# Performance work log

Measured on AMD Instinct MI355X. Metric: run time of the kernel, lower is better.

Reference implementation:

```python
import jax, jax.numpy as jnp
import numpy as np

D_MODEL = 1024
N_HEADS = 16
HEAD_DIM = D_MODEL // N_HEADS


def setup_inputs() -> dict:
    key = jax.random.key(0)
    k_x, k_qkv, k_out = jax.random.split(key, 3)
    B, T = 4, 2048
    x = jax.random.normal(k_x, (B, T, D_MODEL), dtype=jnp.float32)
    # Linear(bias=False): y = x @ W, with W stored as [in, out]
    W_qkv = jax.random.normal(k_qkv, (D_MODEL, 3 * D_MODEL), dtype=jnp.float32) * (D_MODEL ** -0.5)
    W_out = jax.random.normal(k_out, (D_MODEL, D_MODEL), dtype=jnp.float32) * (D_MODEL ** -0.5)
    return {"x": x, "W_qkv": W_qkv, "W_out": W_out}


def reference(x, W_qkv, W_out):
    B, T, C = x.shape
    H, Dh = N_HEADS, HEAD_DIM
    scale = 1.0 / jnp.sqrt(jnp.asarray(Dh, dtype=x.dtype))

    qkv = x @ W_qkv  # [B,T,3C]
    q, k, v = jnp.split(qkv, 3, axis=-1)

    def split_heads(t):
        return t.reshape(B, T, H, Dh).transpose(0, 2, 1, 3)  # [B,H,T,Dh]

    q, k, v = split_heads(q), split_heads(k), split_heads(v)

    scores = jnp.einsum('bhqd,bhkd->bhqk', q, k) * scale  # [B,H,T,T]
    causal = jnp.tril(jnp.ones((T, T), dtype=bool))
    scores = jnp.where(causal, scores, jnp.asarray(-jnp.inf, dtype=scores.dtype))
    attn = jax.nn.softmax(scores, axis=-1)
    # dropout p=0.0 -> identity
    out = jnp.einsum('bhqk,bhkd->bhqd', attn, v)  # [B,H,T,Dh]
    out = out.transpose(0, 2, 1, 3).reshape(B, T, C)
    return out @ W_out
```

## Files before the change

kernel.cpp:

```cpp
#include <hip/hip_runtime.h>
#include <stdint.h>

typedef unsigned short u16;
typedef float f32x4 __attribute__((ext_vector_type(4)));
typedef short s16x8 __attribute__((ext_vector_type(8)));

#define SEQ 2048
#define DM 1024
#define NH 16
#define HD 64
#define BATCH 4
#define ROWS (BATCH*SEQ)

__device__ __forceinline__ u16 f32_bf16(float f) {
  union { float f; uint32_t u; } c; c.f = f;
  uint32_t u = c.u;
  return (u16)((u + 0x7fffu + ((u >> 16) & 1u)) >> 16);
}
__device__ __forceinline__ u16 f32_bf16_trunc(float f) {
  union { float f; uint32_t u; } c; c.f = f;
  return (u16)(c.u >> 16);
}

#define GLOAD_LDS16(g, l) __builtin_amdgcn_global_load_lds( \
    (__attribute__((address_space(1))) void*)(g),           \
    (__attribute__((address_space(3))) void*)(l), 16, 0, 0)

__global__ __launch_bounds__(256) void cast_bf16_k(const float* __restrict__ in,
                                                   u16* __restrict__ out, int n4) {
  int i = blockIdx.x * 256 + threadIdx.x;
  if (i >= n4) return;
  float4 v = ((const float4*)in)[i];
  ushort4 o;
  o.x = f32_bf16(v.x); o.y = f32_bf16(v.y); o.z = f32_bf16(v.z); o.w = f32_bf16(v.w);
  ((ushort4*)out)[i] = o;
}

__global__ __launch_bounds__(256) void cast_transpose_k(const float* __restrict__ in,
                                                        u16* __restrict__ out, int R, int C) {
  __shared__ float tile[32][33];
  int c0 = blockIdx.x * 32, r0 = blockIdx.y * 32;
  int t = threadIdx.x;
  int lr = t >> 3, lc = (t & 7) * 4;
  float4 v = *(const float4*)(in + (size_t)(r0 + lr) * C + c0 + lc);
  tile[lr][lc] = v.x; tile[lr][lc + 1] = v.y; tile[lr][lc + 2] = v.z; tile[lr][lc + 3] = v.w;
  __syncthreads();
  ushort4 o;
  o.x = f32_bf16(tile[lc + 0][lr]);
  o.y = f32_bf16(tile[lc + 1][lr]);
  o.z = f32_bf16(tile[lc + 2][lr]);
  o.w = f32_bf16(tile[lc + 3][lr]);
  *(ushort4*)(out + (size_t)(c0 + lr) * R + r0 + lc) = o;
}

#define QSCALE 0.18033688011112042f


__device__ __forceinline__ f32x4 mfma16(s16x8 a, s16x8 b, f32x4 c) {
  return __builtin_amdgcn_mfma_f32_16x16x32_bf16(a, b, c, 0, 0, 0);
}

template<int STG, int ENDVM, int LAST>
__device__ __forceinline__ void tile_step(
    const u16* lAc, const u16* lBc,
    const u16* lAn, const u16* lBn,
    u16* lAs, u16* lBs,
    const u16* gA0, const u16* gA1, const u16* gB0, const u16* gB1,
    int d0, int d1, int aoff, int boff,
    s16x8 (&fa)[4], s16x8 (&fb)[4],
    s16x8 (&na)[4], s16x8 (&nb)[4],
    f32x4 (&acc)[8][4])
{
  __builtin_amdgcn_s_barrier();
  __builtin_amdgcn_sched_barrier(0);
  s16x8 f1[4];
#pragma unroll
  for (int mi = 0; mi < 4; ++mi) f1[mi] = *(const s16x8*)&lAc[aoff + 2048 + mi * 512];
  if (STG) { GLOAD_LDS16(gA0, lAs + d0); GLOAD_LDS16(gA1, lAs + d1); }
  asm volatile("s_waitcnt lgkmcnt(4)" ::: "memory");
  __builtin_amdgcn_sched_barrier(0);
  __builtin_amdgcn_s_setprio(1);
#pragma unroll
  for (int mi = 0; mi < 4; ++mi)
#pragma unroll
    for (int ni = 0; ni < 4; ++ni)
      acc[mi][ni] = mfma16(fa[mi], fb[ni], acc[mi][ni]);
  __builtin_amdgcn_s_setprio(0);
  __builtin_amdgcn_sched_barrier(0);
  if (STG) { GLOAD_LDS16(gB0, lBs + d0); GLOAD_LDS16(gB1, lBs + d1); }
  if (ENDVM == 8)      asm volatile("s_waitcnt vmcnt(8)" ::: "memory");
  else if (ENDVM == 4) asm volatile("s_waitcnt vmcnt(4)" ::: "memory");
  else if (ENDVM == 0) asm volatile("s_waitcnt vmcnt(0)" ::: "memory");
  __builtin_amdgcn_s_barrier();
  __builtin_amdgcn_sched_barrier(0);
  if (!LAST) {
#pragma unroll
    for (int ni = 0; ni < 4; ++ni) nb[ni] = *(const s16x8*)&lBn[boff + ni * 512];
#pragma unroll
    for (int mi = 0; mi < 4; ++mi) na[mi] = *(const s16x8*)&lAn[aoff + mi * 512];
    asm volatile("s_waitcnt lgkmcnt(8)" ::: "memory");
  } else {
    asm volatile("s_waitcnt lgkmcnt(0)" ::: "memory");
  }
  __builtin_amdgcn_sched_barrier(0);
  __builtin_amdgcn_s_setprio(1);
#pragma unroll
  for (int mi = 0; mi < 4; ++mi)
#pragma unroll
    for (int ni = 0; ni < 4; ++ni)
      acc[4 + mi][ni] = mfma16(f1[mi], fb[ni], acc[4 + mi][ni]);
  __builtin_amdgcn_s_setprio(0);
  __builtin_amdgcn_sched_barrier(0);
}

__global__ __launch_bounds__(512, 2) void qkv_gemm(
    const u16* __restrict__ A, const u16* __restrict__ Bt,
    u16* __restrict__ Qo, u16* __restrict__ Ko, u16* __restrict__ Vo)
{
  __shared__ u16 lA[4][8192];
  __shared__ u16 lB[4][8192];
  int t = threadIdx.x;

  int flat = blockIdx.y * 12 + blockIdx.x;
  int swz = (flat & 7) * 48 + (flat >> 3);
  int by = swz / 12, bx = swz - by * 12;
  int m0 = by * 256, n0 = bx * 256;

  int lane = t & 63, w = t >> 6;
  int m16 = lane & 15, quad = lane >> 4;
  int wm = w >> 2, wn = w & 3;

  int r0 = t >> 2;
  int scol = ((t & 3) ^ ((t >> 3) & 3)) * 8;
  const u16* Ag0 = A  + (size_t)(m0 + r0) * DM + scol;
  const u16* Ag1 = A  + (size_t)(m0 + 128 + r0) * DM + scol;
  const u16* Bg0 = Bt + (size_t)(n0 + r0) * DM + scol;
  const u16* Bg1 = Bt + (size_t)(n0 + 128 + r0) * DM + scol;
  int d0 = t * 8, d1 = 4096 + t * 8;

  int ka = (quad ^ ((m16 >> 1) & 3)) * 8;
  int aoff = (wm * 128 + m16) * 32 + ka;
  int boff = (wn * 64 + m16) * 32 + ka;

  f32x4 acc[8][4];
#pragma unroll
  for (int mi = 0; mi < 8; ++mi)
#pragma unroll
    for (int ni = 0; ni < 4; ++ni)
#pragma unroll
      for (int r = 0; r < 4; ++r) acc[mi][ni][r] = 0.f;

#pragma unroll
  for (int kt = 0; kt < 3; ++kt) {
    GLOAD_LDS16(Ag0 + kt * 32, lA[kt] + d0);
    GLOAD_LDS16(Ag1 + kt * 32, lA[kt] + d1);
    GLOAD_LDS16(Bg0 + kt * 32, lB[kt] + d0);
    GLOAD_LDS16(Bg1 + kt * 32, lB[kt] + d1);
  }
  asm volatile("s_waitcnt vmcnt(8)" ::: "memory");
  __builtin_amdgcn_s_barrier();
  __builtin_amdgcn_sched_barrier(0);

  s16x8 fa0[4], fb0[4], fa1[4], fb1[4];
#pragma unroll
  for (int ni = 0; ni < 4; ++ni) fb0[ni] = *(const s16x8*)&lB[0][boff + ni * 512];
#pragma unroll
  for (int mi = 0; mi < 4; ++mi) fa0[mi] = *(const s16x8*)&lA[0][aoff + mi * 512];

  for (int it = 0; it < 14; ++it) {
    int T = 2 * it;
    tile_step<1, 8, 0>(lA[T & 3], lB[T & 3], lA[(T + 1) & 3], lB[(T + 1) & 3],
                       lA[(T + 3) & 3], lB[(T + 3) & 3],
                       Ag0 + (T + 3) * 32, Ag1 + (T + 3) * 32,
                       Bg0 + (T + 3) * 32, Bg1 + (T + 3) * 32,
                       d0, d1, aoff, boff, fa0, fb0, fa1, fb1, acc);
    tile_step<1, 8, 0>(lA[(T + 1) & 3], lB[(T + 1) & 3], lA[(T + 2) & 3], lB[(T + 2) & 3],
                       lA[(T + 4) & 3], lB[(T + 4) & 3],
                       Ag0 + (T + 4) * 32, Ag1 + (T + 4) * 32,
                       Bg0 + (T + 4) * 32, Bg1 + (T + 4) * 32,
                       d0, d1, aoff, boff, fa1, fb1, fa0, fb0, acc);
  }
  tile_step<1, 8, 0>(lA[0], lB[0], lA[1], lB[1], lA[3], lB[3],
                     Ag0 + 31 * 32, Ag1 + 31 * 32, Bg0 + 31 * 32, Bg1 + 31 * 32,
                     d0, d1, aoff, boff, fa0, fb0, fa1, fb1, acc);
  tile_step<0, 4, 0>(lA[1], lB[1], lA[2], lB[2], lA[0], lB[0],
                     Ag0, Ag1, Bg0, Bg1, d0, d1, aoff, boff, fa1, fb1, fa0, fb0, acc);
  tile_step<0, 0, 0>(lA[2], lB[2], lA[3], lB[3], lA[0], lB[0],
                     Ag0, Ag1, Bg0, Bg1, d0, d1, aoff, boff, fa0, fb0, fa1, fb1, acc);
  tile_step<0, -1, 1>(lA[3], lB[3], lA[0], lB[0], lA[0], lB[0],
                      Ag0, Ag1, Bg0, Bg1, d0, d1, aoff, boff, fa1, fb1, fa0, fb0, acc);

#pragma unroll
  for (int mi = 0; mi < 8; ++mi) {
    int gr = m0 + wm * 128 + mi * 16 + quad * 4;
    int b = gr >> 11, tt = gr & 2047;
#pragma unroll
    for (int ni = 0; ni < 4; ++ni) {
      int gc = n0 + wn * 64 + ni * 16 + m16;
      int sec = gc >> 10, rem = gc & 1023, h = rem >> 6, d = rem & 63;
      if (sec == 0) {
#pragma unroll
        for (int r = 0; r < 4; ++r)
          Qo[(((size_t)b * NH + h) * SEQ + tt + r) * HD + d] = f32_bf16(acc[mi][ni][r] * QSCALE);
      } else if (sec == 1) {
#pragma unroll
        for (int r = 0; r < 4; ++r)
          Ko[(((size_t)b * NH + h) * SEQ + tt + r) * HD + d] = f32_bf16(acc[mi][ni][r]);
      } else {
        ushort4 o;
        o.x = f32_bf16(acc[mi][ni][0]); o.y = f32_bf16(acc[mi][ni][1]);
        o.z = f32_bf16(acc[mi][ni][2]); o.w = f32_bf16(acc[mi][ni][3]);
        *(ushort4*)&Vo[(((size_t)b * NH + h) * HD + d) * SEQ + tt] = o;
      }
    }
  }
}

template<int EPI>
__global__ __launch_bounds__(256) void gemm_bt(
    const u16* __restrict__ A, const u16* __restrict__ Bt,
    float* __restrict__ Cf, u16* __restrict__ Qo, u16* __restrict__ Ko, u16* __restrict__ Vo,
    int M, int N, int K)
{
  __shared__ u16 As[128 * 32];
  __shared__ u16 Bs[128 * 32];
  int t = threadIdx.x;
  int m0 = blockIdx.y * 128, n0 = blockIdx.x * 128;

  int srow = t >> 2, scol8 = (t & 3) * 8;
  const u16* Ag0 = A  + (size_t)(m0 + srow) * K + scol8;
  const u16* Ag1 = A  + (size_t)(m0 + 64 + srow) * K + scol8;
  const u16* Bg0 = Bt + (size_t)(n0 + srow) * K + scol8;
  const u16* Bg1 = Bt + (size_t)(n0 + 64 + srow) * K + scol8;
  u16* Al0 = As + t * 8;  u16* Al1 = As + 2048 + t * 8;
  u16* Bl0 = Bs + t * 8;  u16* Bl1 = Bs + 2048 + t * 8;

  int lane = t & 63, w = t >> 6;
  int m16 = lane & 15, quad = lane >> 4;
  int wr = (w >> 1) * 64, wc = (w & 1) * 64;

  f32x4 acc[4][4];
#pragma unroll
  for (int mi = 0; mi < 4; ++mi)
#pragma unroll
    for (int ni = 0; ni < 4; ++ni)
#pragma unroll
      for (int r = 0; r < 4; ++r) acc[mi][ni][r] = 0.f;

  for (int k0 = 0; k0 < K; k0 += 32) {
    __syncthreads();
    GLOAD_LDS16(Ag0 + k0, Al0);
    GLOAD_LDS16(Ag1 + k0, Al1);
    GLOAD_LDS16(Bg0 + k0, Bl0);
    GLOAD_LDS16(Bg1 + k0, Bl1);
    __syncthreads();
    s16x8 af[4], bf[4];
#pragma unroll
    for (int mi = 0; mi < 4; ++mi)
      af[mi] = *(const s16x8*)(As + (wr + mi * 16 + m16) * 32 + quad * 8);
#pragma unroll
    for (int ni = 0; ni < 4; ++ni)
      bf[ni] = *(const s16x8*)(Bs + (wc + ni * 16 + m16) * 32 + quad * 8);
#pragma unroll
    for (int mi = 0; mi < 4; ++mi)
#pragma unroll
      for (int ni = 0; ni < 4; ++ni)
        acc[mi][ni] = __builtin_amdgcn_mfma_f32_16x16x32_bf16(af[mi], bf[ni], acc[mi][ni], 0, 0, 0);
  }

  if (EPI == 0) {
#pragma unroll
    for (int mi = 0; mi < 4; ++mi) {
      int gr = m0 + wr + mi * 16 + quad * 4;
#pragma unroll
      for (int ni = 0; ni < 4; ++ni) {
        int gc = n0 + wc + ni * 16 + m16;
#pragma unroll
        for (int r = 0; r < 4; ++r)
          Cf[(size_t)(gr + r) * N + gc] = acc[mi][ni][r];
      }
    }
  } else {
#pragma unroll
    for (int mi = 0; mi < 4; ++mi) {
      int gr = m0 + wr + mi * 16 + quad * 4;
      int b = gr >> 11, tt = gr & 2047;
#pragma unroll
      for (int ni = 0; ni < 4; ++ni) {
        int gc = n0 + wc + ni * 16 + m16;
        int sec = gc >> 10, rem = gc & 1023, h = rem >> 6, d = rem & 63;
        if (sec == 0) {
#pragma unroll
          for (int r = 0; r < 4; ++r)
            Qo[(((size_t)b * NH + h) * SEQ + tt + r) * HD + d] = f32_bf16(acc[mi][ni][r] * QSCALE);
        } else if (sec == 1) {
#pragma unroll
          for (int r = 0; r < 4; ++r)
            Ko[(((size_t)b * NH + h) * SEQ + tt + r) * HD + d] = f32_bf16(acc[mi][ni][r]);
        } else {
          ushort4 o;
          o.x = f32_bf16(acc[mi][ni][0]); o.y = f32_bf16(acc[mi][ni][1]);
          o.z = f32_bf16(acc[mi][ni][2]); o.w = f32_bf16(acc[mi][ni][3]);
          *(ushort4*)&Vo[(((size_t)b * NH + h) * HD + d) * SEQ + tt] = o;
        }
      }
    }
  }
}

__global__ __launch_bounds__(256) void attn_k(
    const u16* __restrict__ Q, const u16* __restrict__ K,
    const u16* __restrict__ Vt_g,
    u16* __restrict__ O)
{
  __shared__ u16 Ks[64][72];
  __shared__ u16 Vt[64][72];
  __shared__ u16 Ps[4][32][72];
  int flat = blockIdx.y * 8 + blockIdx.x;
  int xcd = flat & 7, pos = flat >> 3;
  int bh = xcd * 8 + (pos >> 3);
  int xb = pos & 7;
  int t = threadIdx.x, w = t >> 6, lane = t & 63;
  int m16 = lane & 15, quad = lane >> 4;
  int b = bh >> 4, h = bh & 15;

  int srow = t >> 2, sc = (t & 3) * 16;
  const u16* Kg0 = K    + ((size_t)bh * SEQ + srow) * HD  + sc;
  const u16* Vg0 = Vt_g + ((size_t)bh * HD  + srow) * SEQ + sc;

  for (int half = 0; half < 2; ++half) {
    int qt = half ? (15 - xb) : xb;
    int q0 = qt * 128;

    const u16* QbA = Q + ((size_t)bh * SEQ + q0 + w * 32 + m16) * HD + quad * 8;
    s16x8 qA0 = *(const s16x8*)QbA;
    s16x8 qA1 = *(const s16x8*)(QbA + 32);
    s16x8 qB0 = *(const s16x8*)(QbA + 16 * HD);
    s16x8 qB1 = *(const s16x8*)(QbA + 16 * HD + 32);

    f32x4 accA[4], accB[4];
    float lA = 0.f, lB = 0.f;
#pragma unroll
    for (int ni = 0; ni < 4; ++ni)
#pragma unroll
      for (int r = 0; r < 4; ++r) { accA[ni][r] = 0.f; accB[ni][r] = 0.f; }

    int ktmax = 2 * qt + 1;
    for (int kt = 0; kt <= ktmax; ++kt) {
      uint4 kv0 = *(const uint4*)(Kg0 + (size_t)kt * 64 * HD);
      uint4 kv1 = *(const uint4*)(Kg0 + (size_t)kt * 64 * HD + 8);
      uint4 vv0 = *(const uint4*)(Vg0 + kt * 64);
      uint4 vv1 = *(const uint4*)(Vg0 + kt * 64 + 8);
      __syncthreads();
      *(uint4*)&Ks[srow][sc]     = kv0;
      *(uint4*)&Ks[srow][sc + 8] = kv1;
      *(uint4*)&Vt[srow][sc]     = vv0;
      *(uint4*)&Vt[srow][sc + 8] = vv1;
      __syncthreads();

      f32x4 sA[4], sB[4];
#pragma unroll
      for (int ni = 0; ni < 4; ++ni)
#pragma unroll
        for (int r = 0; r < 4; ++r) { sA[ni][r] = 0.f; sB[ni][r] = 0.f; }
#pragma unroll
      for (int ni = 0; ni < 4; ++ni) {
        s16x8 kf0 = *(const s16x8*)&Ks[ni * 16 + m16][quad * 8];
        s16x8 kf1 = *(const s16x8*)&Ks[ni * 16 + m16][32 + quad * 8];
        sA[ni] = mfma16(kf0, qA0, sA[ni]);
        sA[ni] = mfma16(kf1, qA1, sA[ni]);
        sB[ni] = mfma16(kf0, qB0, sB[ni]);
        sB[ni] = mfma16(kf1, qB1, sB[ni]);
      }
      if (kt >= 2 * qt) {
        int qga = q0 + w * 32 + m16;
#pragma unroll
        for (int ni = 0; ni < 4; ++ni) {
          int kb = kt * 64 + ni * 16 + quad * 4;
#pragma unroll
          for (int r = 0; r < 4; ++r) {
            if (kb + r > qga)      sA[ni][r] = -1e30f;
            if (kb + r > qga + 16) sB[ni][r] = -1e30f;
          }
        }
      }

#pragma unroll
      for (int ni = 0; ni < 4; ++ni) {
        ushort4 oA, oB;
#pragma unroll
        for (int r = 0; r < 4; ++r) {
          float pA = __builtin_amdgcn_exp2f(sA[ni][r]);
          float pB = __builtin_amdgcn_exp2f(sB[ni][r]);
          lA += pA; lB += pB;
          ((u16*)&oA)[r] = f32_bf16_trunc(pA);
          ((u16*)&oB)[r] = f32_bf16_trunc(pB);
        }
        *(ushort4*)&Ps[w][m16][ni * 16 + quad * 4]      = oA;
        *(ushort4*)&Ps[w][16 + m16][ni * 16 + quad * 4] = oB;
      }

#pragma unroll
      for (int ks = 0; ks < 2; ++ks) {
        s16x8 pA = *(const s16x8*)&Ps[w][m16][ks * 32 + quad * 8];
        s16x8 pB = *(const s16x8*)&Ps[w][16 + m16][ks * 32 + quad * 8];
#pragma unroll
        for (int ni = 0; ni < 4; ++ni) {
          s16x8 vf = *(const s16x8*)&Vt[ni * 16 + m16][ks * 32 + quad * 8];
          accA[ni] = mfma16(pA, vf, accA[ni]);
          accB[ni] = mfma16(pB, vf, accB[ni]);
        }
      }
    }

    lA += __shfl_xor(lA, 16, 64);
    lA += __shfl_xor(lA, 32, 64);
    lB += __shfl_xor(lB, 16, 64);
    lB += __shfl_xor(lB, 32, 64);

#pragma unroll
    for (int r = 0; r < 4; ++r) {
      int src = (lane & 48) | (quad * 4 + r);
      float la = __shfl(lA, src, 64);
      float lb = __shfl(lB, src, 64);
      float ia = 1.f / la, ib = 1.f / lb;
      int qa = q0 + w * 32 + quad * 4 + r;
      size_t baseA = ((size_t)(b * SEQ + qa)) * DM + h * HD;
      size_t baseB = baseA + (size_t)16 * DM;
#pragma unroll
      for (int ni = 0; ni < 4; ++ni) {
        O[baseA + ni * 16 + m16] = f32_bf16(accA[ni][r] * ia);
        O[baseB + ni * 16 + m16] = f32_bf16(accB[ni][r] * ib);
      }
    }
  }
}

extern "C" void kernel_launch(void* const* d_in, const int* in_sizes, int n_in,
                              void* d_out, int out_size, void* d_ws, size_t ws_size,
                              hipStream_t stream) {
  const float* x    = (const float*)d_in[0];
  const float* Wqkv = (const float*)d_in[1];
  const float* Wout = (const float*)d_in[2];
  float* out = (float*)d_out;

  u16* ws = (u16*)d_ws;
  size_t off = 0;
  u16* x_bf   = ws + off; off += (size_t)ROWS * DM;
  u16* wqkv_t = ws + off; off += (size_t)(3 * DM) * DM;
  u16* wout_t = ws + off; off += (size_t)DM * DM;
  u16* Qb     = ws + off; off += (size_t)BATCH * NH * SEQ * HD;
  u16* Kb     = ws + off; off += (size_t)BATCH * NH * SEQ * HD;
  u16* Vb     = ws + off; off += (size_t)BATCH * NH * SEQ * HD;
  u16* AO     = ws + off; off += (size_t)ROWS * DM;

  cast_bf16_k<<<(ROWS * DM / 4 + 255) / 256, 256, 0, stream>>>(x, x_bf, ROWS * DM / 4);
  cast_transpose_k<<<dim3(3 * DM / 32, DM / 32), 256, 0, stream>>>(Wqkv, wqkv_t, DM, 3 * DM);
  cast_transpose_k<<<dim3(DM / 32, DM / 32), 256, 0, stream>>>(Wout, wout_t, DM, DM);
  qkv_gemm<<<dim3(12, 32), 512, 0, stream>>>(x_bf, wqkv_t, Qb, Kb, Vb);
  attn_k<<<dim3(8, BATCH * NH), 256, 0, stream>>>(Qb, Kb, Vb, AO);
  gemm_bt<0><<<dim3(DM / 128, ROWS / 128), 256, 0, stream>>>(
      AO, wout_t, out, nullptr, nullptr, nullptr, ROWS, DM, DM);
}
```

Before: 259.6 us.

## Widen QKV GEMM tile to 256x384 with three-stage LDS pipeline

The QKV projection GEMM tile grows from 256x256 to 256x384, so each wave computes a 128x96 subtile (8x6 MFMA blocks). The grid shrinks from 384 to 256 workgroups, which matches the 256 CUs with a single wave of blocks instead of 1.5 waves. To fit the larger B tile in LDS, the pipeline drops from four stages to three, with adjusted vmcnt/lgkmcnt waits and an unrolled six-step rotation. In exchange it uses more accumulator registers and has shallower prefetch, which risks exposing load latency and lowering occupancy.

```diff
diff --git a/kernel.cpp b/kernel.cpp
--- a/kernel.cpp
+++ b/kernel.cpp
@@ -65,11 +65,12 @@
     const u16* lAc, const u16* lBc,
     const u16* lAn, const u16* lBn,
     u16* lAs, u16* lBs,
-    const u16* gA0, const u16* gA1, const u16* gB0, const u16* gB1,
-    int d0, int d1, int aoff, int boff,
-    s16x8 (&fa)[4], s16x8 (&fb)[4],
-    s16x8 (&na)[4], s16x8 (&nb)[4],
-    f32x4 (&acc)[8][4])
+    const u16* gA0, const u16* gA1,
+    const u16* gB0, const u16* gB1, const u16* gB2,
+    int d0, int d1, int e2, int aoff, int boff,
+    s16x8 (&fa)[4], s16x8 (&fb)[6],
+    s16x8 (&na)[4], s16x8 (&nb)[6],
+    f32x4 (&acc)[8][6])
 {
   __builtin_amdgcn_s_barrier();
   __builtin_amdgcn_sched_barrier(0);
@@ -83,22 +84,21 @@
 #pragma unroll
   for (int mi = 0; mi < 4; ++mi)
 #pragma unroll
-    for (int ni = 0; ni < 4; ++ni)
+    for (int ni = 0; ni < 6; ++ni)
       acc[mi][ni] = mfma16(fa[mi], fb[ni], acc[mi][ni]);
   __builtin_amdgcn_s_setprio(0);
   __builtin_amdgcn_sched_barrier(0);
-  if (STG) { GLOAD_LDS16(gB0, lBs + d0); GLOAD_LDS16(gB1, lBs + d1); }
-  if (ENDVM == 8)      asm volatile("s_waitcnt vmcnt(8)" ::: "memory");
-  else if (ENDVM == 4) asm volatile("s_waitcnt vmcnt(4)" ::: "memory");
+  if (STG) { GLOAD_LDS16(gB0, lBs + d0); GLOAD_LDS16(gB1, lBs + d1); GLOAD_LDS16(gB2, lBs + e2); }
+  if (ENDVM == 5)      asm volatile("s_waitcnt vmcnt(5)" ::: "memory");
   else if (ENDVM == 0) asm volatile("s_waitcnt vmcnt(0)" ::: "memory");
   __builtin_amdgcn_s_barrier();
   __builtin_amdgcn_sched_barrier(0);
   if (!LAST) {
 #pragma unroll
-    for (int ni = 0; ni < 4; ++ni) nb[ni] = *(const s16x8*)&lBn[boff + ni * 512];
+    for (int ni = 0; ni < 6; ++ni) nb[ni] = *(const s16x8*)&lBn[boff + ni * 512];
 #pragma unroll
     for (int mi = 0; mi < 4; ++mi) na[mi] = *(const s16x8*)&lAn[aoff + mi * 512];
-    asm volatile("s_waitcnt lgkmcnt(8)" ::: "memory");
+    asm volatile("s_waitcnt lgkmcnt(10)" ::: "memory");
   } else {
     asm volatile("s_waitcnt lgkmcnt(0)" ::: "memory");
   }
@@ -107,7 +107,7 @@
 #pragma unroll
   for (int mi = 0; mi < 4; ++mi)
 #pragma unroll
-    for (int ni = 0; ni < 4; ++ni)
+    for (int ni = 0; ni < 6; ++ni)
       acc[4 + mi][ni] = mfma16(f1[mi], fb[ni], acc[4 + mi][ni]);
   __builtin_amdgcn_s_setprio(0);
   __builtin_amdgcn_sched_barrier(0);
@@ -117,14 +117,14 @@
     const u16* __restrict__ A, const u16* __restrict__ Bt,
     u16* __restrict__ Qo, u16* __restrict__ Ko, u16* __restrict__ Vo)
 {
-  __shared__ u16 lA[4][8192];
-  __shared__ u16 lB[4][8192];
+  __shared__ u16 lA[3][8192];
+  __shared__ u16 lB[3][12288];
   int t = threadIdx.x;
 
-  int flat = blockIdx.y * 12 + blockIdx.x;
-  int swz = (flat & 7) * 48 + (flat >> 3);
-  int by = swz / 12, bx = swz - by * 12;
-  int m0 = by * 256, n0 = bx * 256;
+  int flat = blockIdx.y * 8 + blockIdx.x;
+  int swz = (flat & 7) * 32 + (flat >> 3);
+  int by = swz >> 3, bx = swz & 7;
+  int m0 = by * 256, n0 = bx * 384;
 
   int lane = t & 63, w = t >> 6;
   int m16 = lane & 15, quad = lane >> 4;
@@ -136,67 +136,81 @@
   const u16* Ag1 = A  + (size_t)(m0 + 128 + r0) * DM + scol;
   const u16* Bg0 = Bt + (size_t)(n0 + r0) * DM + scol;
   const u16* Bg1 = Bt + (size_t)(n0 + 128 + r0) * DM + scol;
-  int d0 = t * 8, d1 = 4096 + t * 8;
+  const u16* Bg2 = Bt + (size_t)(n0 + 256 + r0) * DM + scol;
+  int d0 = t * 8, d1 = 4096 + t * 8, e2 = 8192 + t * 8;
 
   int ka = (quad ^ ((m16 >> 1) & 3)) * 8;
   int aoff = (wm * 128 + m16) * 32 + ka;
-  int boff = (wn * 64 + m16) * 32 + ka;
-
-  f32x4 acc[8][4];
+  int boff = (wn * 96 + m16) * 32 + ka;
+
+  f32x4 acc[8][6];
 #pragma unroll
   for (int mi = 0; mi < 8; ++mi)
 #pragma unroll
-    for (int ni = 0; ni < 4; ++ni)
+    for (int ni = 0; ni < 6; ++ni)
 #pragma unroll
       for (int r = 0; r < 4; ++r) acc[mi][ni][r] = 0.f;
 
 #pragma unroll
-  for (int kt = 0; kt < 3; ++kt) {
+  for (int kt = 0; kt < 2; ++kt) {
     GLOAD_LDS16(Ag0 + kt * 32, lA[kt] + d0);
     GLOAD_LDS16(Ag1 + kt * 32, lA[kt] + d1);
     GLOAD_LDS16(Bg0 + kt * 32, lB[kt] + d0);
     GLOAD_LDS16(Bg1 + kt * 32, lB[kt] + d1);
-  }
-  asm volatile("s_waitcnt vmcnt(8)" ::: "memory");
+    GLOAD_LDS16(Bg2 + kt * 32, lB[kt] + e2);
+  }
+  asm volatile("s_waitcnt vmcnt(5)" ::: "memory");
   __builtin_amdgcn_s_barrier();
   __builtin_amdgcn_sched_barrier(0);
 
-  s16x8 fa0[4], fb0[4], fa1[4], fb1[4];
-#pragma unroll
-  for (int ni = 0; ni < 4; ++ni) fb0[ni] = *(const s16x8*)&lB[0][boff + ni * 512];
+  s16x8 fa0[4], fa1[4];
+  s16x8 fb0[6], fb1[6];
+#pragma unroll
+  for (int ni = 0; ni < 6; ++ni) fb0[ni] = *(const s16x8*)&lB[0][boff + ni * 512];
 #pragma unroll
   for (int mi = 0; mi < 4; ++mi) fa0[mi] = *(const s16x8*)&lA[0][aoff + mi * 512];
 
-  for (int it = 0; it < 14; ++it) {
-    int T = 2 * it;
-    tile_step<1, 8, 0>(lA[T & 3], lB[T & 3], lA[(T + 1) & 3], lB[(T + 1) & 3],
-                       lA[(T + 3) & 3], lB[(T + 3) & 3],
+  for (int it = 0; it < 5; ++it) {
+    int T = 6 * it;
+    tile_step<1, 5, 0>(lA[0], lB[0], lA[1], lB[1], lA[2], lB[2],
+                       Ag0 + (T + 2) * 32, Ag1 + (T + 2) * 32,
+                       Bg0 + (T + 2) * 32, Bg1 + (T + 2) * 32, Bg2 + (T + 2) * 32,
+                       d0, d1, e2, aoff, boff, fa0, fb0, fa1, fb1, acc);
+    tile_step<1, 5, 0>(lA[1], lB[1], lA[2], lB[2], lA[0], lB[0],
                        Ag0 + (T + 3) * 32, Ag1 + (T + 3) * 32,
-                       Bg0 + (T + 3) * 32, Bg1 + (T + 3) * 32,
-                       d0, d1, aoff, boff, fa0, fb0, fa1, fb1, acc);
-    tile_step<1, 8, 0>(lA[(T + 1) & 3], lB[(T + 1) & 3], lA[(T + 2) & 3], lB[(T + 2) & 3],
-                       lA[(T + 4) & 3], lB[(T + 4) & 3],
+                       Bg0 + (T + 3) * 32, Bg1 + (T + 3) * 32, Bg2 + (T + 3) * 32,
+                       d0, d1, e2, aoff, boff, fa1, fb1, fa0, fb0, acc);
+    tile_step<1, 5, 0>(lA[2], lB[2], lA[0], lB[0], lA[1], lB[1],
                        Ag0 + (T + 4) * 32, Ag1 + (T + 4) * 32,
-                       Bg0 + (T + 4) * 32, Bg1 + (T + 4) * 32,
-                       d0, d1, aoff, boff, fa1, fb1, fa0, fb0, acc);
-  }
-  tile_step<1, 8, 0>(lA[0], lB[0], lA[1], lB[1], lA[3], lB[3],
-                     Ag0 + 31 * 32, Ag1 + 31 * 32, Bg0 + 31 * 32, Bg1 + 31 * 32,
-                     d0, d1, aoff, boff, fa0, fb0, fa1, fb1, acc);
-  tile_step<0, 4, 0>(lA[1], lB[1], lA[2], lB[2], lA[0], lB[0],
-                     Ag0, Ag1, Bg0, Bg1, d0, d1, aoff, boff, fa1, fb1, fa0, fb0, acc);
-  tile_step<0, 0, 0>(lA[2], lB[2], lA[3], lB[3], lA[0], lB[0],
-                     Ag0, Ag1, Bg0, Bg1, d0, d1, aoff, boff, fa0, fb0, fa1, fb1, acc);
-  tile_step<0, -1, 1>(lA[3], lB[3], lA[0], lB[0], lA[0], lB[0],
-                      Ag0, Ag1, Bg0, Bg1, d0, d1, aoff, boff, fa1, fb1, fa0, fb0, acc);
+                       Bg0 + (T + 4) * 32, Bg1 + (T + 4) * 32, Bg2 + (T + 4) * 32,
+                       d0, d1, e2, aoff, boff, fa0, fb0, fa1, fb1, acc);
+    tile_step<1, 5, 0>(lA[0], lB[0], lA[1], lB[1], lA[2], lB[2],
+                       Ag0 + (T + 5) * 32, Ag1 + (T + 5) * 32,
+                       Bg0 + (T + 5) * 32, Bg1 + (T + 5) * 32, Bg2 + (T + 5) * 32,
+                       d0, d1, e2, aoff, boff, fa1, fb1, fa0, fb0, acc);
+    tile_step<1, 5, 0>(lA[1], lB[1], lA[2], lB[2], lA[0], lB[0],
+                       Ag0 + (T + 6) * 32, Ag1 + (T + 6) * 32,
+                       Bg0 + (T + 6) * 32, Bg1 + (T + 6) * 32, Bg2 + (T + 6) * 32,
+                       d0, d1, e2, aoff, boff, fa0, fb0, fa1, fb1, acc);
+    tile_step<1, 5, 0>(lA[2], lB[2], lA[0], lB[0], lA[1], lB[1],
+                       Ag0 + (T + 7) * 32, Ag1 + (T + 7) * 32,
+                       Bg0 + (T + 7) * 32, Bg1 + (T + 7) * 32, Bg2 + (T + 7) * 32,
+                       d0, d1, e2, aoff, boff, fa1, fb1, fa0, fb0, acc);
+  }
+  tile_step<0, 0, 0>(lA[0], lB[0], lA[1], lB[1], lA[2], lB[2],
+                     Ag0, Ag1, Bg0, Bg1, Bg2,
+                     d0, d1, e2, aoff, boff, fa0, fb0, fa1, fb1, acc);
+  tile_step<0, -1, 1>(lA[1], lB[1], lA[2], lB[2], lA[0], lB[0],
+                      Ag0, Ag1, Bg0, Bg1, Bg2,
+                      d0, d1, e2, aoff, boff, fa1, fb1, fa0, fb0, acc);
 
 #pragma unroll
   for (int mi = 0; mi < 8; ++mi) {
     int gr = m0 + wm * 128 + mi * 16 + quad * 4;
     int b = gr >> 11, tt = gr & 2047;
 #pragma unroll
-    for (int ni = 0; ni < 4; ++ni) {
-      int gc = n0 + wn * 64 + ni * 16 + m16;
+    for (int ni = 0; ni < 6; ++ni) {
+      int gc = n0 + wn * 96 + ni * 16 + m16;
       int sec = gc >> 10, rem = gc & 1023, h = rem >> 6, d = rem & 63;
       if (sec == 0) {
 #pragma unroll
@@ -457,7 +471,7 @@
   cast_bf16_k<<<(ROWS * DM / 4 + 255) / 256, 256, 0, stream>>>(x, x_bf, ROWS * DM / 4);
   cast_transpose_k<<<dim3(3 * DM / 32, DM / 32), 256, 0, stream>>>(Wqkv, wqkv_t, DM, 3 * DM);
   cast_transpose_k<<<dim3(DM / 32, DM / 32), 256, 0, stream>>>(Wout, wout_t, DM, DM);
-  qkv_gemm<<<dim3(12, 32), 512, 0, stream>>>(x_bf, wqkv_t, Qb, Kb, Vb);
+  qkv_gemm<<<dim3(8, 32), 512, 0, stream>>>(x_bf, wqkv_t, Qb, Kb, Vb);
   attn_k<<<dim3(8, BATCH * NH), 256, 0, stream>>>(Qb, Kb, Vb, AO);
   gemm_bt<0><<<dim3(DM / 128, ROWS / 128), 256, 0, stream>>>(
       AO, wout_t, out, nullptr, nullptr, nullptr, ROWS, DM, DM);
```

After: 393.9 us. 1.52x slower.

## Double-buffer K/V tiles in LDS with register prefetch in attention

Applied to the files above, without the earlier changes.

Doubles the shared-memory K and V tiles and keeps the next tile's global loads in registers while the current tile is processed. The next tile is written into the alternate buffer after compute, and the global loads for the tile after that are issued right away. This is meant to hide global load latency behind the MFMA and softmax work. It costs extra LDS, which may lower occupancy, and adds register pressure from the in-flight prefetch.

```diff
diff --git a/kernel.cpp b/kernel.cpp
--- a/kernel.cpp
+++ b/kernel.cpp
@@ -313,8 +313,8 @@
     const u16* __restrict__ Vt_g,
     u16* __restrict__ O)
 {
-  __shared__ u16 Ks[64][72];
-  __shared__ u16 Vt[64][72];
+  __shared__ u16 Ks[2][64][72];
+  __shared__ u16 Vt[2][64][72];
   __shared__ u16 Ps[4][32][72];
   int flat = blockIdx.y * 8 + blockIdx.x;
   int xcd = flat & 7, pos = flat >> 3;
@@ -346,17 +346,24 @@
       for (int r = 0; r < 4; ++r) { accA[ni][r] = 0.f; accB[ni][r] = 0.f; }
 
     int ktmax = 2 * qt + 1;
+
+    uint4 kv0 = *(const uint4*)(Kg0);
+    uint4 kv1 = *(const uint4*)(Kg0 + 8);
+    uint4 vv0 = *(const uint4*)(Vg0);
+    uint4 vv1 = *(const uint4*)(Vg0 + 8);
+    __syncthreads();
+    *(uint4*)&Ks[0][srow][sc]     = kv0;
+    *(uint4*)&Ks[0][srow][sc + 8] = kv1;
+    *(uint4*)&Vt[0][srow][sc]     = vv0;
+    *(uint4*)&Vt[0][srow][sc + 8] = vv1;
+    kv0 = *(const uint4*)(Kg0 + (size_t)64 * HD);
+    kv1 = *(const uint4*)(Kg0 + (size_t)64 * HD + 8);
+    vv0 = *(const uint4*)(Vg0 + 64);
+    vv1 = *(const uint4*)(Vg0 + 64 + 8);
+    __syncthreads();
+
     for (int kt = 0; kt <= ktmax; ++kt) {
-      uint4 kv0 = *(const uint4*)(Kg0 + (size_t)kt * 64 * HD);
-      uint4 kv1 = *(const uint4*)(Kg0 + (size_t)kt * 64 * HD + 8);
-      uint4 vv0 = *(const uint4*)(Vg0 + kt * 64);
-      uint4 vv1 = *(const uint4*)(Vg0 + kt * 64 + 8);
-      __syncthreads();
-      *(uint4*)&Ks[srow][sc]     = kv0;
-      *(uint4*)&Ks[srow][sc + 8] = kv1;
-      *(uint4*)&Vt[srow][sc]     = vv0;
-      *(uint4*)&Vt[srow][sc + 8] = vv1;
-      __syncthreads();
+      int cur = kt & 1;
 
       f32x4 sA[4], sB[4];
 #pragma unroll
@@ -365,8 +372,8 @@
         for (int r = 0; r < 4; ++r) { sA[ni][r] = 0.f; sB[ni][r] = 0.f; }
 #pragma unroll
       for (int ni = 0; ni < 4; ++ni) {
-        s16x8 kf0 = *(const s16x8*)&Ks[ni * 16 + m16][quad * 8];
-        s16x8 kf1 = *(const s16x8*)&Ks[ni * 16 + m16][32 + quad * 8];
+        s16x8 kf0 = *(const s16x8*)&Ks[cur][ni * 16 + m16][quad * 8];
+        s16x8 kf1 = *(const s16x8*)&Ks[cur][ni * 16 + m16][32 + quad * 8];
         sA[ni] = mfma16(kf0, qA0, sA[ni]);
         sA[ni] = mfma16(kf1, qA1, sA[ni]);
         sB[ni] = mfma16(kf0, qB0, sB[ni]);
@@ -406,10 +413,26 @@
         s16x8 pB = *(const s16x8*)&Ps[w][16 + m16][ks * 32 + quad * 8];
 #pragma unroll
         for (int ni = 0; ni < 4; ++ni) {
-          s16x8 vf = *(const s16x8*)&Vt[ni * 16 + m16][ks * 32 + quad * 8];
+          s16x8 vf = *(const s16x8*)&Vt[cur][ni * 16 + m16][ks * 32 + quad * 8];
           accA[ni] = mfma16(pA, vf, accA[ni]);
           accB[ni] = mfma16(pB, vf, accB[ni]);
         }
+      }
+
+      if (kt < ktmax) {
+        int nxt = (kt + 1) & 1;
+        __syncthreads();
+        *(uint4*)&Ks[nxt][srow][sc]     = kv0;
+        *(uint4*)&Ks[nxt][srow][sc + 8] = kv1;
+        *(uint4*)&Vt[nxt][srow][sc]     = vv0;
+        *(uint4*)&Vt[nxt][srow][sc + 8] = vv1;
+        if (kt + 2 <= ktmax) {
+          kv0 = *(const uint4*)(Kg0 + (size_t)(kt + 2) * 64 * HD);
+          kv1 = *(const uint4*)(Kg0 + (size_t)(kt + 2) * 64 * HD + 8);
+          vv0 = *(const uint4*)(Vg0 + (kt + 2) * 64);
+          vv1 = *(const uint4*)(Vg0 + (kt + 2) * 64 + 8);
+        }
+        __syncthreads();
       }
     }
 
```

Measured after the change: 284.0 us. 9.4% more time.
